# Kernel tuning notes

Hardware: AMD Instinct MI355X
Metric: run time of the kernel (lower is better)

## Reference

```python
import jax, jax.numpy as jnp
import numpy as np

# Mamba-1.4B-like dims
BATCH, SEQ, HID = 1, 2048, 2048
INTER, STATE, DT_RANK, KCONV = 4096, 16, 128, 4


def setup_inputs() -> dict:
    key = jax.random.key(0)
    ks = jax.random.split(key, 8)
    f = jnp.float32
    return {
        "input_states": jax.random.normal(ks[0], (BATCH, SEQ, HID), f),
        "in_proj_w": jax.random.normal(ks[1], (HID, 2 * INTER), f) * (HID ** -0.5),
        "conv_w": jax.random.normal(ks[2], (INTER, 1, KCONV), f) * (KCONV ** -0.5),  # (O, I/groups=1, K) depthwise
        "conv_b": jnp.zeros((INTER,), f),
        "x_proj_w": jax.random.normal(ks[3], (INTER, DT_RANK + 2 * STATE), f) * (INTER ** -0.5),
        "dt_proj_w": jax.random.normal(ks[4], (DT_RANK, INTER), f) * (DT_RANK ** -0.5),
        "dt_proj_b": jax.random.normal(ks[5], (INTER,), f) * 0.1,
        "A_log": jnp.log(jnp.broadcast_to(jnp.arange(1, STATE + 1, dtype=f), (INTER, STATE))),
        "D": jnp.ones((INTER,), f),
        "out_proj_w": jax.random.normal(ks[6], (INTER, HID), f) * (INTER ** -0.5),
    }


def _mamba_forward(input_states, in_proj_w, conv_w, conv_b, x_proj_w,
                   dt_proj_w, dt_proj_b, A_log, D, out_proj_w):
    Bsz, L, _ = input_states.shape
    Idim, _, K = conv_w.shape
    N = A_log.shape[1]
    R = dt_proj_w.shape[0]

    proj = input_states @ in_proj_w                       # (B, L, 2I)
    hidden, gate = jnp.split(proj, 2, axis=-1)            # each (B, L, I)

    # depthwise causal conv over sequence (pad K-1, keep first L outputs)
    xc = jnp.swapaxes(hidden, 1, 2)                       # (B, I, L)
    xc = jax.lax.conv_general_dilated(
        xc, conv_w, window_strides=(1,), padding=((K - 1, K - 1),),
        feature_group_count=Idim)
    xc = xc[:, :, :L] + conv_b[None, :, None]
    u = jax.nn.silu(jnp.swapaxes(xc, 1, 2))               # (B, L, I)

    # input-dependent SSM params
    ssm_in = u @ x_proj_w                                 # (B, L, R + 2N)
    dt_in, Bc, Cc = jnp.split(ssm_in, [R, R + N], axis=-1)
    dt = jax.nn.softplus(dt_in @ dt_proj_w + dt_proj_b)   # (B, L, I)
    A = -jnp.exp(A_log)                                   # (I, N)

    def step(state, xs):
        dt_t, B_t, C_t, u_t = xs                          # (B,I) (B,N) (B,N) (B,I)
        dA = jnp.exp(dt_t[:, :, None] * A[None])          # (B, I, N)
        state = state * dA + (dt_t * u_t)[:, :, None] * B_t[:, None, :]
        y_t = jnp.einsum('bin,bn->bi', state, C_t)
        return state, y_t

    xs = (jnp.swapaxes(dt, 0, 1), jnp.swapaxes(Bc, 0, 1),
          jnp.swapaxes(Cc, 0, 1), jnp.swapaxes(u, 0, 1))
    state0 = jnp.zeros((Bsz, Idim, N), dt.dtype)
    _, ys = jax.lax.scan(step, state0, xs)                # (L, B, I)
    y = jnp.swapaxes(ys, 0, 1)                            # (B, L, I)

    y = (y + u * D) * jax.nn.silu(gate)
    return y @ out_proj_w                                 # (B, L, H)


def reference(input_states, in_proj_w, conv_w, conv_b, x_proj_w,
              dt_proj_w, dt_proj_b, A_log, D, out_proj_w):
    return _mamba_forward(input_states, in_proj_w, conv_w, conv_b, x_proj_w,
                          dt_proj_w, dt_proj_b, A_log, D, out_proj_w)
```

## Files before the change

kernel.cpp:

```cpp
#include <hip/hip_runtime.h>
#include <stdint.h>

#define LSEQ 2048
#define HID  2048
#define IDIM 4096
#define NSTATE 16
#define RRANK 128
#define GDIM 160

#define GCHUNK 64
#define TCHUNK (LSEQ / GCHUNK)

typedef _Float16 f16x8 __attribute__((ext_vector_type(8)));
typedef _Float16 f16x2 __attribute__((ext_vector_type(2)));
typedef float f32x4 __attribute__((ext_vector_type(4)));

#define GLOAD_LDS16(g, l) __builtin_amdgcn_global_load_lds( \
    (const __attribute__((address_space(1))) void*)(g),     \
    (__attribute__((address_space(3))) void*)(l), 16, 0, 0)

__device__ __forceinline__ float softplus_f(float x) {
    if (x > 20.f) return x;
    return log1pf(__expf(x));
}
__device__ __forceinline__ float silu_f(float x) {
    return x / (1.f + __expf(-x));
}

__device__ __forceinline__ void transpose_tile(const float* __restrict__ in,
                                               _Float16* __restrict__ out,
                                               int R, int C, int tr, int tc,
                                               _Float16 (*tile)[66], int t) {
    const int c0 = tc * 64, r0 = tr * 64;
    const int tx = t & 15, ty = t >> 4;
    const int ox = t & 7, oy = t >> 3;
    const bool full = (c0 + 64 <= C) && (r0 + 64 <= R);
    if (full) {
        #pragma unroll
        for (int j = 0; j < 4; ++j) {
            int r = ty + j * 16;
            float4 v = *(const float4*)(in + (long)(r0 + r) * C + c0 + tx * 4);
            tile[r][tx * 4 + 0] = (_Float16)v.x;
            tile[r][tx * 4 + 1] = (_Float16)v.y;
            tile[r][tx * 4 + 2] = (_Float16)v.z;
            tile[r][tx * 4 + 3] = (_Float16)v.w;
        }
        __syncthreads();
        #pragma unroll
        for (int j = 0; j < 2; ++j) {
            int c = oy + j * 32;
            f16x8 v;
            #pragma unroll
            for (int e = 0; e < 8; ++e) v[e] = tile[ox * 8 + e][c];
            *(f16x8*)(out + (long)(c0 + c) * R + r0 + ox * 8) = v;
        }
    } else {
        #pragma unroll
        for (int j = 0; j < 4; ++j) {
            int r = ty + j * 16;
            #pragma unroll
            for (int e = 0; e < 4; ++e) {
                int c = c0 + tx * 4 + e;
                float v = (r0 + r < R && c < C) ? in[(long)(r0 + r) * C + c] : 0.f;
                tile[r][tx * 4 + e] = (_Float16)v;
            }
        }
        __syncthreads();
        #pragma unroll
        for (int j = 0; j < 2; ++j) {
            int c = c0 + oy + j * 32;
            if (c < C) {
                #pragma unroll
                for (int e = 0; e < 8; ++e) {
                    int r = r0 + ox * 8 + e;
                    if (r < R) out[(long)c * R + r] = tile[ox * 8 + e][oy + j * 32];
                }
            }
        }
    }
}

__global__ __launch_bounds__(256)
void prep_kernel(const float* __restrict__ x_in, const float* __restrict__ w_in,
                 _Float16* __restrict__ Xf, _Float16* __restrict__ Wt1) {
    __shared__ _Float16 tile[64][66];
    int b = blockIdx.x;
    if (b < 4096) { transpose_tile(w_in, Wt1, HID, 2 * IDIM, b / 128, b % 128, tile, threadIdx.x); return; }
    b -= 4096;
    long base = (long)b * 4096 + threadIdx.x * 16;
    #pragma unroll
    for (int h = 0; h < 2; ++h) {
        float4 a = *(const float4*)(x_in + base + h * 8);
        float4 c = *(const float4*)(x_in + base + h * 8 + 4);
        f16x8 v;
        v[0] = (_Float16)a.x; v[1] = (_Float16)a.y; v[2] = (_Float16)a.z; v[3] = (_Float16)a.w;
        v[4] = (_Float16)c.x; v[5] = (_Float16)c.y; v[6] = (_Float16)c.z; v[7] = (_Float16)c.w;
        *(f16x8*)(Xf + base + h * 8) = v;
    }
}

#define BM 128
#define BK 64

template <typename CT, bool SOFTPLUS>
__device__ __forceinline__
void gemm_core(const _Float16* __restrict__ A, const _Float16* __restrict__ Bt,
               CT* __restrict__ C, int M, int N, int K, int kc,
               const float* __restrict__ bias,
               _Float16* __restrict__ As, _Float16* __restrict__ Bs,
               int m0, int n0, int zz) {
    const int t = threadIdx.x;
    const int wave = t >> 6;
    const int lane = t & 63;
    const int wm = wave >> 1, wn = wave & 1;
    const int lrow = lane & 15;
    const int quad = lane >> 4;
    const int sw8 = (lrow & 7) * 8;

    f32x4 acc[4][4];
    #pragma unroll
    for (int mi = 0; mi < 4; ++mi)
        #pragma unroll
        for (int ni = 0; ni < 4; ++ni)
            #pragma unroll
            for (int r = 0; r < 4; ++r)
                acc[mi][ni][r] = 0.f;

    const int k_begin = zz * kc;
    const _Float16* pA[4];
    const _Float16* pB[4];
    #pragma unroll
    for (int j = 0; j < 4; ++j) {
        int s = j * 256 + t;
        int row = s >> 3;
        int ch = (s & 7) ^ (row & 7);
        pA[j] = A + (long)(m0 + row) * K + ch * 8 + k_begin;
        pB[j] = Bt + (long)(n0 + row) * K + ch * 8 + k_begin;
    }

    for (int kk = 0; kk < kc; kk += BK) {
        #pragma unroll
        for (int j = 0; j < 4; ++j) {
            GLOAD_LDS16(pA[j], As + (j * 256 + wave * 64) * 8);
            pA[j] += BK;
            GLOAD_LDS16(pB[j], Bs + (j * 256 + wave * 64) * 8);
            pB[j] += BK;
        }
        __syncthreads();

        #pragma unroll
        for (int h = 0; h < 2; ++h) {
            const int qoff = (h * 32 + quad * 8) ^ sw8;
            f16x8 af[4], bf[4];
            #pragma unroll
            for (int mi = 0; mi < 4; ++mi)
                af[mi] = *(const f16x8*)(As + (wm * 64 + mi * 16 + lrow) * BK + qoff);
            #pragma unroll
            for (int ni = 0; ni < 4; ++ni)
                bf[ni] = *(const f16x8*)(Bs + (wn * 64 + ni * 16 + lrow) * BK + qoff);
            #pragma unroll
            for (int mi = 0; mi < 4; ++mi)
                #pragma unroll
                for (int ni = 0; ni < 4; ++ni)
                    acc[mi][ni] = __builtin_amdgcn_mfma_f32_16x16x32_f16(af[mi], bf[ni], acc[mi][ni], 0, 0, 0);
        }
        __syncthreads();
    }

    CT* Cz = C + (long)zz * M * N;
    #pragma unroll
    for (int mi = 0; mi < 4; ++mi) {
        #pragma unroll
        for (int ni = 0; ni < 4; ++ni) {
            int col = n0 + wn * 64 + ni * 16 + lrow;
            if (col < N) {
                float bv = SOFTPLUS ? bias[col] : 0.f;
                #pragma unroll
                for (int r = 0; r < 4; ++r) {
                    int row = m0 + wm * 64 + mi * 16 + quad * 4 + r;
                    float v = acc[mi][ni][r];
                    if (SOFTPLUS) v = softplus_f(v + bv);
                    Cz[(long)row * N + col] = (CT)v;
                }
            }
        }
    }
}

template <typename CT, bool SOFTPLUS>
__global__ __launch_bounds__(256)
void gemm_bt_kernel(const _Float16* __restrict__ A, const _Float16* __restrict__ Bt,
                    CT* __restrict__ C, int M, int N, int K, int kc,
                    const float* __restrict__ bias) {
    __shared__ _Float16 As[BM * BK];
    __shared__ _Float16 Bs[128 * BK];
    gemm_core<CT, SOFTPLUS>(A, Bt, C, M, N, K, kc, bias, As, Bs,
                            blockIdx.y * BM, blockIdx.x * 128, blockIdx.z);
}

template <typename CT>
__device__ __forceinline__
void gemm256_core(const _Float16* __restrict__ A, const _Float16* __restrict__ Bt,
                  CT* __restrict__ C, int M, int N, int K, int kc,
                  int m0, int n0, int zz, _Float16* __restrict__ sm) {
    const int t = threadIdx.x;
    const int wave = t >> 6, lane = t & 63;
    const int wm = wave >> 2, wn = wave & 3;
    const int lrow = lane & 15, quad = lane >> 4;
    const int ns = kc >> 5;

    const int rA = t >> 2;
    const int qe = (((t & 3) ^ (rA & 3)) * 8);
    const _Float16* gA0 = A  + (size_t)(m0 + rA) * K + (size_t)zz * kc + qe;
    const _Float16* gA1 = gA0 + (size_t)128 * K;
    const _Float16* gB0 = Bt + (size_t)(n0 + rA) * K + (size_t)zz * kc + qe;
    const _Float16* gB1 = gB0 + (size_t)128 * K;

    _Float16* const bsm = sm + 32768;
    const int dA = wave * 512;

    f32x4 acc[8][4];
    #pragma unroll
    for (int mi = 0; mi < 8; ++mi)
        #pragma unroll
        for (int ni = 0; ni < 4; ++ni)
            #pragma unroll
            for (int r = 0; r < 4; ++r) acc[mi][ni][r] = 0.f;

    #define ISSUE_SLICE(slot) do {                                          \
        _Float16* as_ = sm  + (slot) * 8192;                                \
        _Float16* bs_ = bsm + (slot) * 8192;                                \
        GLOAD_LDS16(gA0, as_ + dA);                                         \
        GLOAD_LDS16(gA1, as_ + 4096 + dA);                                  \
        GLOAD_LDS16(gB0, bs_ + dA);                                         \
        GLOAD_LDS16(gB1, bs_ + 4096 + dA);                                  \
        gA0 += 32; gA1 += 32; gB0 += 32; gB1 += 32;                         \
    } while (0)

    ISSUE_SLICE(0); ISSUE_SLICE(1); ISSUE_SLICE(2);
    asm volatile("s_waitcnt vmcnt(8)" ::: "memory");
    __builtin_amdgcn_s_barrier();
    __builtin_amdgcn_sched_barrier(0);

    const int arow0 = (wm * 128 + lrow) * 32;
    const int brow0 = (wn * 64 + lrow) * 32;
    const int koff  = ((quad ^ (lrow & 3)) * 8);

    for (int s2 = 0; s2 < ns; ++s2) {
        const _Float16* as_ = sm  + (s2 & 3) * 8192;
        const _Float16* bs_ = bsm + (s2 & 3) * 8192;
        if (s2 + 3 < ns) ISSUE_SLICE((s2 + 3) & 3);
        __builtin_amdgcn_sched_barrier(0);

        f16x8 af[8], bf[4];
        #pragma unroll
        for (int mi = 0; mi < 8; ++mi)
            af[mi] = *(const f16x8*)(as_ + arow0 + mi * 512 + koff);
        #pragma unroll
        for (int ni = 0; ni < 4; ++ni)
            bf[ni] = *(const f16x8*)(bs_ + brow0 + ni * 512 + koff);

        __builtin_amdgcn_s_setprio(1);
        #pragma unroll
        for (int mi = 0; mi < 8; ++mi)
            #pragma unroll
            for (int ni = 0; ni < 4; ++ni)
                acc[mi][ni] = __builtin_amdgcn_mfma_f32_16x16x32_f16(af[mi], bf[ni], acc[mi][ni], 0, 0, 0);
        __builtin_amdgcn_s_setprio(0);

        if (s2 + 1 < ns) {
            if (s2 + 4 <= ns)      asm volatile("s_waitcnt vmcnt(8)" ::: "memory");
            else if (s2 + 3 == ns) asm volatile("s_waitcnt vmcnt(4)" ::: "memory");
            else                   asm volatile("s_waitcnt vmcnt(0)" ::: "memory");
            __builtin_amdgcn_s_barrier();
            __builtin_amdgcn_sched_barrier(0);
        }
    }
    #undef ISSUE_SLICE

    CT* Cz = C + (size_t)zz * ((size_t)M * N);
    const int crow = m0 + wm * 128 + quad * 4;
    const int ccol = n0 + wn * 64 + lrow;
    #pragma unroll
    for (int mi = 0; mi < 8; ++mi)
        #pragma unroll
        for (int ni = 0; ni < 4; ++ni)
            #pragma unroll
            for (int r = 0; r < 4; ++r)
                Cz[(size_t)(crow + mi * 16 + r) * N + ccol + ni * 16] = (CT)acc[mi][ni][r];
}

__global__ __launch_bounds__(512, 2)
void gemm256_kernel(const _Float16* __restrict__ A, const _Float16* __restrict__ Bt,
                    float* __restrict__ C, int M, int N, int K, int kc) {
    __shared__ _Float16 sm[65536];
    int nb = gridDim.x * gridDim.y * gridDim.z;
    int f0 = blockIdx.x + gridDim.x * (blockIdx.y + gridDim.y * blockIdx.z);
    int cpx = nb >> 3;
    int f = (f0 & 7) * cpx + (f0 >> 3);
    int bx = f % gridDim.x;
    int r2 = f / gridDim.x;
    int by = r2 % gridDim.y;
    int bz = r2 / gridDim.y;
    gemm256_core<float>(A, Bt, C, M, N, K, kc, by * 256, bx * 256, bz, sm);
}

__global__ __launch_bounds__(512, 2)
void inproj_plus_kernel(const _Float16* __restrict__ Xf, const _Float16* __restrict__ Wt1,
                        _Float16* __restrict__ proj,
                        const float* __restrict__ xw, const float* __restrict__ dtw,
                        const float* __restrict__ ow,
                        _Float16* __restrict__ Wt2, _Float16* __restrict__ Wt3,
                        _Float16* __restrict__ Wt4) {
    __shared__ _Float16 sm[65536];
    int b = blockIdx.x;
    if (b < 256) {
        int f = (b & 7) * 32 + (b >> 3);
        gemm256_core<_Float16>(Xf, Wt1, proj, LSEQ, 2 * IDIM, HID, HID,
                               (f >> 5) * 256, (f & 31) * 256, 0, sm);
        return;
    }
    b -= 256;
    const int half = threadIdx.x >> 8;
    const int tid  = threadIdx.x & 255;
    int tile_idx = b * 2 + half;
    _Float16 (*tile)[66] = (_Float16 (*)[66])(sm + half * 4224);
    if (tile_idx < 192) {
        transpose_tile(xw, Wt2, IDIM, GDIM, tile_idx / 3, tile_idx % 3, tile, tid);
    } else if (tile_idx < 320) {
        int j = tile_idx - 192;
        transpose_tile(dtw, Wt3, RRANK, IDIM, j / 64, j % 64, tile, tid);
    } else {
        int j = tile_idx - 320;
        transpose_tile(ow, Wt4, IDIM, HID, j / 32, j % 32, tile, tid);
    }
}

__global__ void xproj_reduce_kernel(const float* __restrict__ part, float* __restrict__ ssm,
                                    _Float16* __restrict__ dtin) {
    int idx = blockIdx.x * 256 + threadIdx.x;
    if (idx >= LSEQ * GDIM) return;
    int t = idx / GDIM;
    int c = idx - t * GDIM;
    float v = 0.f;
    #pragma unroll
    for (int k = 0; k < 16; ++k)
        v += part[((long)k * LSEQ + t) * 256 + c];
    ssm[idx] = v;
    if (c < RRANK) dtin[t * RRANK + c] = (_Float16)v;
}

__global__ void opart_reduce_kernel(const float* __restrict__ part, float* __restrict__ out) {
    size_t base = ((size_t)blockIdx.x * 256 + threadIdx.x) * 32;
    const size_t SL = (size_t)LSEQ * HID;
    #pragma unroll
    for (int j = 0; j < 8; ++j) {
        float4 a = *(const float4*)(part + base + j * 4);
        float4 b = *(const float4*)(part + SL + base + j * 4);
        float4 c = *(const float4*)(part + 2 * SL + base + j * 4);
        float4 d = *(const float4*)(part + 3 * SL + base + j * 4);
        float4 o = make_float4(a.x + b.x + c.x + d.x,
                               a.y + b.y + c.y + d.y,
                               a.z + b.z + c.z + d.z,
                               a.w + b.w + c.w + d.w);
        *(float4*)(out + base + j * 4) = o;
    }
}

__global__ void conv_silu_kernel(const _Float16* __restrict__ proj, const float* __restrict__ w,
                                 const float* __restrict__ b, _Float16* __restrict__ u16) {
    int idx = blockIdx.x * 256 + threadIdx.x;
    int i0 = (idx & 511) * 8;
    int t0 = (idx >> 9) * 4;
    f16x8 r[7];
    #pragma unroll
    for (int k = 0; k < 7; ++k) {
        int tt = t0 - 3 + k;
        if (tt >= 0) r[k] = *(const f16x8*)(proj + (long)tt * (2 * IDIM) + i0);
        else         r[k] = f16x8{0,0,0,0,0,0,0,0};
    }
    float4 wv[8]; float bb[8];
    #pragma unroll
    for (int j = 0; j < 8; ++j) { wv[j] = ((const float4*)w)[i0 + j]; bb[j] = b[i0 + j]; }
    #pragma unroll
    for (int tt = 0; tt < 4; ++tt) {
        f16x8 res;
        #pragma unroll
        for (int j = 0; j < 8; ++j) {
            float a = bb[j] + (float)r[tt][j] * wv[j].x + (float)r[tt+1][j] * wv[j].y
                            + (float)r[tt+2][j] * wv[j].z + (float)r[tt+3][j] * wv[j].w;
            res[j] = (_Float16)(a / (1.f + __expf(-a)));
        }
        *(f16x8*)(u16 + (long)(t0 + tt) * IDIM + i0) = res;
    }
}

__global__ __launch_bounds__(256)
void scan_pass1_kernel(const _Float16* __restrict__ dtf, const float* __restrict__ ssm,
                       const _Float16* __restrict__ u16, const float* __restrict__ A_log,
                       _Float16* __restrict__ Pc, _Float16* __restrict__ Sc) {
    const int c = blockIdx.y;
    const int i0 = (blockIdx.x * 256 + threadIdx.x) * 2;

    __shared__ float Bs[TCHUNK * 16];
    for (int idx = threadIdx.x; idx < TCHUNK * 16; idx += 256) {
        int t = idx >> 4, n = idx & 15;
        Bs[idx] = ssm[(c * TCHUNK + t) * GDIM + RRANK + n];
    }
    __syncthreads();

    float A[2][16];
    #pragma unroll
    for (int ch = 0; ch < 2; ++ch) {
        const float4* Ap = (const float4*)(A_log + (long)(i0 + ch) * 16);
        #pragma unroll
        for (int q = 0; q < 4; ++q) {
            float4 v = Ap[q];
            A[ch][q * 4 + 0] = -__expf(v.x);
            A[ch][q * 4 + 1] = -__expf(v.y);
            A[ch][q * 4 + 2] = -__expf(v.z);
            A[ch][q * 4 + 3] = -__expf(v.w);
        }
    }

    float s[2][16];
    float sumdt[2] = {0.f, 0.f};
    #pragma unroll
    for (int ch = 0; ch < 2; ++ch)
        #pragma unroll
        for (int n = 0; n < 16; ++n) s[ch][n] = 0.f;

    long base = (long)c * TCHUNK * IDIM + i0;
    for (int t = 0; t < TCHUNK; ++t) {
        f16x2 dt2 = *(const f16x2*)(dtf + base + (long)t * IDIM);
        f16x2 u2  = *(const f16x2*)(u16 + base + (long)t * IDIM);
        #pragma unroll
        for (int ch = 0; ch < 2; ++ch) {
            float dt = (float)dt2[ch];
            float dtu = dt * (float)u2[ch];
            sumdt[ch] += dt;
            #pragma unroll
            for (int n = 0; n < 16; ++n) {
                float dA = __expf(dt * A[ch][n]);
                s[ch][n] = s[ch][n] * dA + dtu * Bs[t * 16 + n];
            }
        }
    }

    long o = ((long)c * IDIM + i0) * 16;
    #pragma unroll
    for (int ch = 0; ch < 2; ++ch) {
        #pragma unroll
        for (int q = 0; q < 2; ++q) {
            f16x8 pv, sv;
            #pragma unroll
            for (int e = 0; e < 8; ++e) {
                pv[e] = (_Float16)__expf(A[ch][q * 8 + e] * sumdt[ch]);
                sv[e] = (_Float16)s[ch][q * 8 + e];
            }
            *(f16x8*)(Pc + o + ch * 16 + q * 8) = pv;
            *(f16x8*)(Sc + o + ch * 16 + q * 8) = sv;
        }
    }
}

__global__ void scan_combine_kernel(const _Float16* __restrict__ Pc, _Float16* __restrict__ ScInit) {
    int tid = blockIdx.x * 256 + threadIdx.x;
    const long stride = (long)IDIM * 16;
    const long off = (long)tid * 2;
    f16x2 p4[4], s4[4];
    #pragma unroll
    for (int k = 0; k < 4; ++k) {
        p4[k] = *(const f16x2*)(Pc + (long)k * stride + off);
        s4[k] = *(const f16x2*)(ScInit + (long)k * stride + off);
    }
    float c0 = 0.f, c1 = 0.f;
    for (int g = 0; g < GCHUNK / 4; ++g) {
        f16x2 pc[4], sc[4];
        #pragma unroll
        for (int k = 0; k < 4; ++k) { pc[k] = p4[k]; sc[k] = s4[k]; }
        if (g + 1 < GCHUNK / 4) {
            #pragma unroll
            for (int k = 0; k < 4; ++k) {
                long o2 = (long)((g + 1) * 4 + k) * stride + off;
                p4[k] = *(const f16x2*)(Pc + o2);
                s4[k] = *(const f16x2*)(ScInit + o2);
            }
        }
        #pragma unroll
        for (int k = 0; k < 4; ++k) {
            long o = (long)(g * 4 + k) * stride + off;
            *(f16x2*)(ScInit + o) = f16x2{(_Float16)c0, (_Float16)c1};
            c0 = c0 * (float)pc[k][0] + (float)sc[k][0];
            c1 = c1 * (float)pc[k][1] + (float)sc[k][1];
        }
    }
}

__global__ __launch_bounds__(256)
void scan_pass3_kernel(const _Float16* __restrict__ dtf, const float* __restrict__ ssm,
                       const _Float16* __restrict__ u16, const _Float16* __restrict__ proj,
                       const float* __restrict__ A_log, const float* __restrict__ Dp,
                       const _Float16* __restrict__ Init, _Float16* __restrict__ y16) {
    const int c = blockIdx.y;
    const int i0 = (blockIdx.x * 256 + threadIdx.x) * 2;

    __shared__ float Bs[TCHUNK * 16];
    __shared__ float Cs[TCHUNK * 16];
    for (int idx = threadIdx.x; idx < TCHUNK * 16; idx += 256) {
        int t = idx >> 4, n = idx & 15;
        Bs[idx] = ssm[(c * TCHUNK + t) * GDIM + RRANK + n];
        Cs[idx] = ssm[(c * TCHUNK + t) * GDIM + RRANK + NSTATE + n];
    }
    __syncthreads();

    float A[2][16];
    #pragma unroll
    for (int ch = 0; ch < 2; ++ch) {
        const float4* Ap = (const float4*)(A_log + (long)(i0 + ch) * 16);
        #pragma unroll
        for (int q = 0; q < 4; ++q) {
            float4 v = Ap[q];
            A[ch][q * 4 + 0] = -__expf(v.x);
            A[ch][q * 4 + 1] = -__expf(v.y);
            A[ch][q * 4 + 2] = -__expf(v.z);
            A[ch][q * 4 + 3] = -__expf(v.w);
        }
    }
    float2 Dv = *(const float2*)(Dp + i0);

    float s[2][16];
    {
        long o = ((long)c * IDIM + i0) * 16;
        #pragma unroll
        for (int ch = 0; ch < 2; ++ch)
            #pragma unroll
            for (int q = 0; q < 2; ++q) {
                f16x8 v = *(const f16x8*)(Init + o + ch * 16 + q * 8);
                #pragma unroll
                for (int e = 0; e < 8; ++e) s[ch][q * 8 + e] = (float)v[e];
            }
    }

    long base = (long)c * TCHUNK * IDIM + i0;
    for (int t = 0; t < TCHUNK; ++t) {
        f16x2 dt2 = *(const f16x2*)(dtf + base + (long)t * IDIM);
        f16x2 u2  = *(const f16x2*)(u16 + base + (long)t * IDIM);
        int tg = c * TCHUNK + t;
        f16x2 g2 = *(const f16x2*)(proj + (long)tg * (2 * IDIM) + IDIM + i0);
        f16x2 res;
        #pragma unroll
        for (int ch = 0; ch < 2; ++ch) {
            float dt = (float)dt2[ch];
            float uv = (float)u2[ch];
            float dtu = dt * uv;
            float y = 0.f;
            #pragma unroll
            for (int n = 0; n < 16; ++n) {
                float dA = __expf(dt * A[ch][n]);
                s[ch][n] = s[ch][n] * dA + dtu * Bs[t * 16 + n];
                y += s[ch][n] * Cs[t * 16 + n];
            }
            float g = (float)g2[ch];
            float Dch = ch ? Dv.y : Dv.x;
            res[ch] = (_Float16)((y + uv * Dch) * silu_f(g));
        }
        *(f16x2*)(y16 + base + (long)t * IDIM) = res;
    }
}

extern "C" void kernel_launch(void* const* d_in, const int* in_sizes, int n_in,
                              void* d_out, int out_size, void* d_ws, size_t ws_size,
                              hipStream_t stream) {
    const float* x_in  = (const float*)d_in[0];
    const float* w_in  = (const float*)d_in[1];
    const float* cw    = (const float*)d_in[2];
    const float* cb    = (const float*)d_in[3];
    const float* xw    = (const float*)d_in[4];
    const float* dtw   = (const float*)d_in[5];
    const float* dtb   = (const float*)d_in[6];
    const float* alog  = (const float*)d_in[7];
    const float* Dp    = (const float*)d_in[8];
    const float* ow    = (const float*)d_in[9];
    float* out = (float*)d_out;

    char* p = (char*)d_ws;
    auto alloc = [&](size_t bytes) { char* r = p; p += (bytes + 255) & ~255ull; return r; };
    _Float16* Xf    = (_Float16*)alloc((size_t)LSEQ * HID * 2);
    _Float16* Wt1   = (_Float16*)alloc((size_t)2 * IDIM * HID * 2);
    _Float16* proj  = (_Float16*)alloc((size_t)LSEQ * 2 * IDIM * 2);
    _Float16* u16   = (_Float16*)alloc((size_t)LSEQ * IDIM * 2);
    _Float16* Wt2   = (_Float16*)alloc((size_t)256 * IDIM * 2);
    float*    ssm   = (float*)alloc((size_t)LSEQ * GDIM * 4);
    _Float16* dtin  = (_Float16*)alloc((size_t)LSEQ * RRANK * 2);
    _Float16* Wt3   = (_Float16*)alloc((size_t)IDIM * RRANK * 2);
    _Float16* dtf   = (_Float16*)alloc((size_t)LSEQ * IDIM * 2);
    _Float16* Wt4   = (_Float16*)alloc((size_t)HID * IDIM * 2);
    _Float16* y16   = (_Float16*)alloc((size_t)LSEQ * IDIM * 2);

    float* xpart = (float*)Wt1;
    _Float16* Pc = (_Float16*)Wt1;
    _Float16* Sc = Pc + (size_t)GCHUNK * IDIM * 16;
    float* opart32 = (float*)proj;

    prep_kernel<<<5120, 256, 0, stream>>>(x_in, w_in, Xf, Wt1);
    inproj_plus_kernel<<<256 + 1184, 512, 0, stream>>>(
        Xf, Wt1, proj, xw, dtw, ow, Wt2, Wt3, Wt4);
    conv_silu_kernel<<<(LSEQ / 4) * (IDIM / 8) / 256, 256, 0, stream>>>(proj, cw, cb, u16);
    gemm_bt_kernel<float, false><<<dim3(2, LSEQ / BM, 16), 256, 0, stream>>>(
        u16, Wt2, xpart, LSEQ, 256, IDIM, IDIM / 16, nullptr);
    xproj_reduce_kernel<<<(LSEQ * GDIM + 255) / 256, 256, 0, stream>>>(xpart, ssm, dtin);
    gemm_bt_kernel<_Float16, true><<<dim3(IDIM / 128, LSEQ / BM, 1), 256, 0, stream>>>(
        dtin, Wt3, dtf, LSEQ, IDIM, RRANK, RRANK, dtb);
    scan_pass1_kernel<<<dim3(IDIM / 512, GCHUNK), 256, 0, stream>>>(
        dtf, ssm, u16, alog, Pc, Sc);
    scan_combine_kernel<<<(IDIM * NSTATE / 2) / 256, 256, 0, stream>>>(Pc, Sc);
    scan_pass3_kernel<<<dim3(IDIM / 512, GCHUNK), 256, 0, stream>>>(
        dtf, ssm, u16, proj, alog, Dp, Sc, y16);
    gemm256_kernel<<<dim3(HID / 256, LSEQ / 256, 4), 512, 0, stream>>>(
        y16, Wt4, opart32, LSEQ, HID, IDIM, IDIM / 4);
    opart_reduce_kernel<<<(LSEQ * HID / 32) / 256, 256, 0, stream>>>(opart32, out);
}
```

Before: 473.7 us.

## Move weight transposes into prep kernel and re-swizzle 256-tile GEMM LDS layout

```diff
diff --git a/kernel.cpp b/kernel.cpp
--- a/kernel.cpp
+++ b/kernel.cpp
@@ -82,21 +82,34 @@
 
 __global__ __launch_bounds__(256)
 void prep_kernel(const float* __restrict__ x_in, const float* __restrict__ w_in,
-                 _Float16* __restrict__ Xf, _Float16* __restrict__ Wt1) {
+                 const float* __restrict__ xw, const float* __restrict__ dtw,
+                 const float* __restrict__ ow,
+                 _Float16* __restrict__ Xf, _Float16* __restrict__ Wt1,
+                 _Float16* __restrict__ Wt2, _Float16* __restrict__ Wt3,
+                 _Float16* __restrict__ Wt4) {
     __shared__ _Float16 tile[64][66];
     int b = blockIdx.x;
     if (b < 4096) { transpose_tile(w_in, Wt1, HID, 2 * IDIM, b / 128, b % 128, tile, threadIdx.x); return; }
     b -= 4096;
-    long base = (long)b * 4096 + threadIdx.x * 16;
-    #pragma unroll
-    for (int h = 0; h < 2; ++h) {
-        float4 a = *(const float4*)(x_in + base + h * 8);
-        float4 c = *(const float4*)(x_in + base + h * 8 + 4);
-        f16x8 v;
-        v[0] = (_Float16)a.x; v[1] = (_Float16)a.y; v[2] = (_Float16)a.z; v[3] = (_Float16)a.w;
-        v[4] = (_Float16)c.x; v[5] = (_Float16)c.y; v[6] = (_Float16)c.z; v[7] = (_Float16)c.w;
-        *(f16x8*)(Xf + base + h * 8) = v;
-    }
+    if (b < 1024) {
+        long base = (long)b * 4096 + threadIdx.x * 16;
+        #pragma unroll
+        for (int h = 0; h < 2; ++h) {
+            float4 a = *(const float4*)(x_in + base + h * 8);
+            float4 c = *(const float4*)(x_in + base + h * 8 + 4);
+            f16x8 v;
+            v[0] = (_Float16)a.x; v[1] = (_Float16)a.y; v[2] = (_Float16)a.z; v[3] = (_Float16)a.w;
+            v[4] = (_Float16)c.x; v[5] = (_Float16)c.y; v[6] = (_Float16)c.z; v[7] = (_Float16)c.w;
+            *(f16x8*)(Xf + base + h * 8) = v;
+        }
+        return;
+    }
+    b -= 1024;
+    if (b < 192) { transpose_tile(xw, Wt2, IDIM, GDIM, b / 3, b % 3, tile, threadIdx.x); return; }
+    b -= 192;
+    if (b < 128) { transpose_tile(dtw, Wt3, RRANK, IDIM, b / 64, b % 64, tile, threadIdx.x); return; }
+    b -= 128;
+    transpose_tile(ow, Wt4, IDIM, HID, b / 32, b % 32, tile, threadIdx.x);
 }
 
 #define BM 128
@@ -209,11 +222,13 @@
     const int lrow = lane & 15, quad = lane >> 4;
     const int ns = kc >> 5;
 
-    const int rA = t >> 2;
-    const int qe = (((t & 3) ^ (rA & 3)) * 8);
-    const _Float16* gA0 = A  + (size_t)(m0 + rA) * K + (size_t)zz * kc + qe;
+    const int l0 = t >> 3;
+    const int e  = (t & 7) ^ (l0 & 7);
+    const int sp = e >> 2, sc = e & 3;
+    const int rowA = 2 * l0 + sp;
+    const _Float16* gA0 = A  + (size_t)(m0 + rowA) * K + (size_t)zz * kc + sc * 8;
     const _Float16* gA1 = gA0 + (size_t)128 * K;
-    const _Float16* gB0 = Bt + (size_t)(n0 + rA) * K + (size_t)zz * kc + qe;
+    const _Float16* gB0 = Bt + (size_t)(n0 + rowA) * K + (size_t)zz * kc + sc * 8;
     const _Float16* gB1 = gB0 + (size_t)128 * K;
 
     _Float16* const bsm = sm + 32768;
@@ -242,9 +257,10 @@
     __builtin_amdgcn_s_barrier();
     __builtin_amdgcn_sched_barrier(0);
 
-    const int arow0 = (wm * 128 + lrow) * 32;
-    const int brow0 = (wn * 64 + lrow) * 32;
-    const int koff  = ((quad ^ (lrow & 3)) * 8);
+    const int hl = lrow >> 1;
+    const int koff = ((quad + 4 * (lrow & 1)) ^ hl) * 8;
+    const int arow0 = wm * 4096 + hl * 64 + koff;
+    const int brow0 = wn * 2048 + hl * 64 + koff;
 
     for (int s2 = 0; s2 < ns; ++s2) {
         const _Float16* as_ = sm  + (s2 & 3) * 8192;
@@ -255,10 +271,10 @@
         f16x8 af[8], bf[4];
         #pragma unroll
         for (int mi = 0; mi < 8; ++mi)
-            af[mi] = *(const f16x8*)(as_ + arow0 + mi * 512 + koff);
+            af[mi] = *(const f16x8*)(as_ + arow0 + mi * 512);
         #pragma unroll
         for (int ni = 0; ni < 4; ++ni)
-            bf[ni] = *(const f16x8*)(bs_ + brow0 + ni * 512 + koff);
+            bf[ni] = *(const f16x8*)(bs_ + brow0 + ni * 512);
 
         __builtin_amdgcn_s_setprio(1);
         #pragma unroll
@@ -306,34 +322,13 @@
 }
 
 __global__ __launch_bounds__(512, 2)
-void inproj_plus_kernel(const _Float16* __restrict__ Xf, const _Float16* __restrict__ Wt1,
-                        _Float16* __restrict__ proj,
-                        const float* __restrict__ xw, const float* __restrict__ dtw,
-                        const float* __restrict__ ow,
-                        _Float16* __restrict__ Wt2, _Float16* __restrict__ Wt3,
-                        _Float16* __restrict__ Wt4) {
+void inproj256_kernel(const _Float16* __restrict__ Xf, const _Float16* __restrict__ Wt1,
+                      _Float16* __restrict__ proj) {
     __shared__ _Float16 sm[65536];
     int b = blockIdx.x;
-    if (b < 256) {
-        int f = (b & 7) * 32 + (b >> 3);
-        gemm256_core<_Float16>(Xf, Wt1, proj, LSEQ, 2 * IDIM, HID, HID,
-                               (f >> 5) * 256, (f & 31) * 256, 0, sm);
-        return;
-    }
-    b -= 256;
-    const int half = threadIdx.x >> 8;
-    const int tid  = threadIdx.x & 255;
-    int tile_idx = b * 2 + half;
-    _Float16 (*tile)[66] = (_Float16 (*)[66])(sm + half * 4224);
-    if (tile_idx < 192) {
-        transpose_tile(xw, Wt2, IDIM, GDIM, tile_idx / 3, tile_idx % 3, tile, tid);
-    } else if (tile_idx < 320) {
-        int j = tile_idx - 192;
-        transpose_tile(dtw, Wt3, RRANK, IDIM, j / 64, j % 64, tile, tid);
-    } else {
-        int j = tile_idx - 320;
-        transpose_tile(ow, Wt4, IDIM, HID, j / 32, j % 32, tile, tid);
-    }
+    int f = (b & 7) * 32 + (b >> 3);
+    gemm256_core<_Float16>(Xf, Wt1, proj, LSEQ, 2 * IDIM, HID, HID,
+                           (f >> 5) * 256, (f & 31) * 256, 0, sm);
 }
 
 __global__ void xproj_reduce_kernel(const float* __restrict__ part, float* __restrict__ ssm,
@@ -603,9 +598,9 @@
     _Float16* Sc = Pc + (size_t)GCHUNK * IDIM * 16;
     float* opart32 = (float*)proj;
 
-    prep_kernel<<<5120, 256, 0, stream>>>(x_in, w_in, Xf, Wt1);
-    inproj_plus_kernel<<<256 + 1184, 512, 0, stream>>>(
-        Xf, Wt1, proj, xw, dtw, ow, Wt2, Wt3, Wt4);
+    prep_kernel<<<7488, 256, 0, stream>>>(x_in, w_in, xw, dtw, ow,
+                                          Xf, Wt1, Wt2, Wt3, Wt4);
+    inproj256_kernel<<<256, 512, 0, stream>>>(Xf, Wt1, proj);
     conv_silu_kernel<<<(LSEQ / 4) * (IDIM / 8) / 256, 256, 0, stream>>>(proj, cw, cb, u16);
     gemm_bt_kernel<float, false><<<dim3(2, LSEQ / BM, 16), 256, 0, stream>>>(
         u16, Wt2, xpart, LSEQ, 256, IDIM, IDIM / 16, nullptr);
```

Result: no change. 474.0 us (+0.1%).
